# Performance work log

Measured on AMD Instinct MI355X. Metric: run time of the kernel, lower is better.

## Reference

```python
import math
import jax, jax.numpy as jnp
import numpy as np

HIDDEN = 768
NUM_HEADS = 12
HEAD_DIM = HIDDEN // NUM_HEADS
WINDOW = 256      # one-sided attention window
DILATION = 1
BATCH = 2
SEQ = 2048


def setup_inputs() -> dict:
    key = jax.random.key(0)
    ks = jax.random.split(key, 7)
    s = 1.0 / math.sqrt(HIDDEN)
    return {
        "hidden_states": jax.random.normal(ks[0], (BATCH, SEQ, HIDDEN), jnp.float32),
        "Wq": jax.random.normal(ks[1], (HIDDEN, HIDDEN), jnp.float32) * s,
        "bq": jnp.zeros((HIDDEN,), jnp.float32),
        "Wk": jax.random.normal(ks[2], (HIDDEN, HIDDEN), jnp.float32) * s,
        "bk": jnp.zeros((HIDDEN,), jnp.float32),
        "Wv": jax.random.normal(ks[3], (HIDDEN, HIDDEN), jnp.float32) * s,
        "bv": jnp.zeros((HIDDEN,), jnp.float32),
    }


def _band_mask(seq_len, dtype):
    # mask[i, j] = 1 iff |j - i| <= WINDOW * DILATION and (j - i) % DILATION == 0
    idx = jnp.arange(seq_len)
    rel = idx[None, :] - idx[:, None]  # [S, S]
    m = (jnp.abs(rel) <= WINDOW * DILATION) & (jnp.mod(rel, DILATION) == 0)
    return m.astype(dtype)


def reference(hidden_states, Wq, bq, Wk, bk, Wv, bv):
    B, S, M = hidden_states.shape
    H, D = NUM_HEADS, HEAD_DIM

    # torch nn.Linear: y = x @ W.T + b; query additionally scaled by 1/sqrt(head_dim)
    q = (hidden_states @ Wq.T + bq) / math.sqrt(D)
    k = hidden_states @ Wk.T + bk
    v = hidden_states @ Wv.T + bv

    # [B, S, M] -> [B, H, S, D]
    q = q.reshape(B, S, H, D).transpose(0, 2, 1, 3)
    k = k.reshape(B, S, H, D).transpose(0, 2, 1, 3)
    v = v.reshape(B, S, H, D).transpose(0, 2, 1, 3)

    # Dense scores, then MULTIPLICATIVE band mask (faithful: scores * mask, not additive -inf)
    scores = jnp.einsum("bhqd,bhkd->bhqk", q, k)
    mask = _band_mask(S, scores.dtype)  # [S, S], broadcasts over B, H
    scores = scores * mask

    probs = jax.nn.softmax(scores, axis=-1)  # [B, H, S, S]
    ctx = jnp.einsum("bhqk,bhkd->bhqd", probs, v)
    return ctx.transpose(0, 2, 1, 3).reshape(B, S, M)
```

## Files before the change

### kernel.cpp

```cpp
#include <hip/hip_runtime.h>
#include <hip/hip_bf16.h>
#include <cstdint>

#define SEQ    2048
#define HIDDEN 768
#define NHEAD  12
#define HDIM   64
#define WIN    256
#define BATCH  2
#define MTOT   (BATCH * SEQ)

typedef __attribute__((ext_vector_type(8))) short short8;
typedef __attribute__((ext_vector_type(4))) float f32x4;

__device__ __forceinline__ ushort bf16_rne(float f) {
    uint u = __float_as_uint(f);
    uint r = u + 0x7FFFu + ((u >> 16) & 1u);
    return (ushort)(r >> 16);
}
__device__ __forceinline__ float bf16_to_f(ushort h) {
    return __uint_as_float(((uint)h) << 16);
}

__global__ __launch_bounds__(256) void proj_mfma_kernel(
    const float* __restrict__ X,
    const float* __restrict__ Wq, const float* __restrict__ bq,
    const float* __restrict__ Wk, const float* __restrict__ bk,
    const float* __restrict__ Wv, const float* __restrict__ bv,
    float* __restrict__ Qo, float* __restrict__ Ko, float* __restrict__ Vo)
{
    const int which = blockIdx.z;
    const float* __restrict__ W    = (which == 0) ? Wq : (which == 1) ? Wk : Wv;
    const float* __restrict__ bias = (which == 0) ? bq : (which == 1) ? bk : bv;
    float* __restrict__ out        = (which == 0) ? Qo : (which == 1) ? Ko : Vo;
    const float scale = (which == 0) ? 0.125f : 1.0f;

    __shared__ __align__(16) ushort Ahi[128 * 64];
    __shared__ __align__(16) ushort Alo[128 * 64];
    __shared__ __align__(16) ushort Bhi[64 * 64];
    __shared__ __align__(16) ushort Blo[64 * 64];

    const int t  = threadIdx.x;
    const int m0 = blockIdx.x * 128;
    const int h  = blockIdx.y;
    const int n0 = h * 64;

    const int w    = t >> 6;
    const int lane = t & 63;
    const int wr   = w >> 1;
    const int wc   = w & 1;
    const int lr   = lane & 15;
    const int lk   = lane >> 4;

    f32x4 acc[4][2];
#pragma unroll
    for (int i = 0; i < 4; ++i)
#pragma unroll
        for (int j = 0; j < 2; ++j) acc[i][j] = (f32x4){0.f, 0.f, 0.f, 0.f};

    for (int k0 = 0; k0 < HIDDEN; k0 += 64) {
        __syncthreads();
#pragma unroll
        for (int i = 0; i < 8; ++i) {
            int id  = t + i * 256;
            int row = id >> 4;
            int c4  = id & 15;
            const float4 xv = *(const float4*)&X[(size_t)(m0 + row) * HIDDEN + k0 + c4 * 4];
            ushort h0 = bf16_rne(xv.x), h1 = bf16_rne(xv.y),
                   h2 = bf16_rne(xv.z), h3 = bf16_rne(xv.w);
            ushort l0 = bf16_rne(xv.x - bf16_to_f(h0)),
                   l1 = bf16_rne(xv.y - bf16_to_f(h1)),
                   l2 = bf16_rne(xv.z - bf16_to_f(h2)),
                   l3 = bf16_rne(xv.w - bf16_to_f(h3));
            int idx = (row * 64 + c4 * 4) ^ ((row & 7) << 3);
            *(uint2*)&Ahi[idx] = make_uint2((uint)h0 | ((uint)h1 << 16),
                                            (uint)h2 | ((uint)h3 << 16));
            *(uint2*)&Alo[idx] = make_uint2((uint)l0 | ((uint)l1 << 16),
                                            (uint)l2 | ((uint)l3 << 16));
        }
#pragma unroll
        for (int i = 0; i < 4; ++i) {
            int id  = t + i * 256;
            int row = id >> 4;
            int c4  = id & 15;
            const float4 wv4 = *(const float4*)&W[(size_t)(n0 + row) * HIDDEN + k0 + c4 * 4];
            ushort h0 = bf16_rne(wv4.x), h1 = bf16_rne(wv4.y),
                   h2 = bf16_rne(wv4.z), h3 = bf16_rne(wv4.w);
            ushort l0 = bf16_rne(wv4.x - bf16_to_f(h0)),
                   l1 = bf16_rne(wv4.y - bf16_to_f(h1)),
                   l2 = bf16_rne(wv4.z - bf16_to_f(h2)),
                   l3 = bf16_rne(wv4.w - bf16_to_f(h3));
            int idx = (row * 64 + c4 * 4) ^ ((row & 7) << 3);
            *(uint2*)&Bhi[idx] = make_uint2((uint)h0 | ((uint)h1 << 16),
                                            (uint)h2 | ((uint)h3 << 16));
            *(uint2*)&Blo[idx] = make_uint2((uint)l0 | ((uint)l1 << 16),
                                            (uint)l2 | ((uint)l3 << 16));
        }
        __syncthreads();

#pragma unroll
        for (int s = 0; s < 2; ++s) {
            short8 ah[4], al[4], bh[2], bl[2];
#pragma unroll
            for (int fm = 0; fm < 4; ++fm) {
                int row = wr * 64 + fm * 16 + lr;
                int idx = (row * 64 + s * 32 + lk * 8) ^ ((row & 7) << 3);
                ah[fm] = *(const short8*)&Ahi[idx];
                al[fm] = *(const short8*)&Alo[idx];
            }
#pragma unroll
            for (int fn = 0; fn < 2; ++fn) {
                int row = wc * 32 + fn * 16 + lr;
                int idx = (row * 64 + s * 32 + lk * 8) ^ ((row & 7) << 3);
                bh[fn] = *(const short8*)&Bhi[idx];
                bl[fn] = *(const short8*)&Blo[idx];
            }
#pragma unroll
            for (int fm = 0; fm < 4; ++fm)
#pragma unroll
                for (int fn = 0; fn < 2; ++fn) {
                    acc[fm][fn] = __builtin_amdgcn_mfma_f32_16x16x32_bf16(
                        ah[fm], bh[fn], acc[fm][fn], 0, 0, 0);
                    acc[fm][fn] = __builtin_amdgcn_mfma_f32_16x16x32_bf16(
                        ah[fm], bl[fn], acc[fm][fn], 0, 0, 0);
                    acc[fm][fn] = __builtin_amdgcn_mfma_f32_16x16x32_bf16(
                        al[fm], bh[fn], acc[fm][fn], 0, 0, 0);
                }
        }
    }

#pragma unroll
    for (int fn = 0; fn < 2; ++fn) {
        int d = wc * 32 + fn * 16 + lr;
        float bval = bias[n0 + d];
#pragma unroll
        for (int fm = 0; fm < 4; ++fm) {
#pragma unroll
            for (int r = 0; r < 4; ++r) {
                int m  = m0 + wr * 64 + fm * 16 + lk * 4 + r;
                int bb = m >> 11;
                int ss = m & (SEQ - 1);
                out[(((size_t)(bb * NHEAD + h) * SEQ) + ss) * HDIM + d] =
                    (acc[fm][fn][r] + bval) * scale;
            }
        }
    }
}

__global__ __launch_bounds__(256) void vprefix_kernel(
    const float* __restrict__ V, float* __restrict__ Vpre)
{
    const int bh    = blockIdx.x;
    const int d     = threadIdx.x & 63;
    const int chunk = threadIdx.x >> 6;
    const float* vb = &V[(size_t)bh * SEQ * HDIM];
    float* pb       = &Vpre[(size_t)bh * SEQ * HDIM];

    __shared__ float csum[4][64];
    const int s0 = chunk * 512;
    float sum = 0.f;
    for (int s = s0; s < s0 + 512; ++s) sum += vb[(size_t)s * HDIM + d];
    csum[chunk][d] = sum;
    __syncthreads();
    float run = 0.f;
    for (int c = 0; c < chunk; ++c) run += csum[c][d];
    for (int s = s0; s < s0 + 512; ++s) {
        run += vb[(size_t)s * HDIM + d];
        pb[(size_t)s * HDIM + d] = run;
    }
}

__global__ __launch_bounds__(256, 3) void attn_kernel(
    const float* __restrict__ Q, const float* __restrict__ K,
    const float* __restrict__ V, const float* __restrict__ Vpre,
    float* __restrict__ out)
{
    __shared__ __align__(16) ushort Khi[64 * 64], Klo[64 * 64];
    __shared__ __align__(16) ushort VThi[64 * 64], VTlo[64 * 64];
    __shared__ __align__(16) ushort Phi_s[4][16 * 64];
    __shared__ __align__(16) ushort Plo_s[4][16 * 64];

    const int t    = threadIdx.x;
    const int lane = t & 63;
    const int wv   = t >> 6;
    const int l15  = lane & 15;
    const int g2   = lane >> 4;

    const int L    = blockIdx.x;
    const int xcd  = L & 7;
    const int slot = L >> 3;
    const int bh   = xcd * 3 + (slot >> 5);
    const int qb   = slot & 31;
    const int b    = bh / NHEAD;
    const int h    = bh % NHEAD;
    const int i0   = qb * 64;
    const int i    = i0 + wv * 16 + l15;

    const float* kbase = &K[(size_t)bh * SEQ * HDIM];
    const float* vbase = &V[(size_t)bh * SEQ * HDIM];

    short8 qh[2], qlo[2];
    {
        const float* qrow = &Q[((size_t)bh * SEQ + i) * HDIM];
#pragma unroll
        for (int s = 0; s < 2; ++s) {
            float4 a = *(const float4*)&qrow[s * 32 + g2 * 8];
            float4 c = *(const float4*)&qrow[s * 32 + g2 * 8 + 4];
            float qf[8] = {a.x, a.y, a.z, a.w, c.x, c.y, c.z, c.w};
#pragma unroll
            for (int j = 0; j < 8; ++j) {
                ushort hh = bf16_rne(qf[j]);
                qh[s][j]  = (short)hh;
                qlo[s][j] = (short)bf16_rne(qf[j] - bf16_to_f(hh));
            }
        }
    }

    const int krow = t >> 2;
    const int kc   = (t & 3) * 16;
    const int vkp  = t >> 3;
    const int vdc  = (t & 7) * 8;
    float4 kpre[4], vp0[2], vp1[2];

    const int jlo_blk = max(0, i0 - WIN);
    const int jhi_blk = min(SEQ - 1, i0 + 63 + WIN);

    auto LOADT = [&](int jt2) {
        const float* kr = &kbase[(size_t)(jt2 + krow) * HDIM + kc];
        kpre[0] = *(const float4*)&kr[0];
        kpre[1] = *(const float4*)&kr[4];
        kpre[2] = *(const float4*)&kr[8];
        kpre[3] = *(const float4*)&kr[12];
        const float* vr0 = &vbase[(size_t)(jt2 + 2 * vkp) * HDIM + vdc];
        const float* vr1 = &vbase[(size_t)(jt2 + 2 * vkp + 1) * HDIM + vdc];
        vp0[0] = *(const float4*)&vr0[0];
        vp0[1] = *(const float4*)&vr0[4];
        vp1[0] = *(const float4*)&vr1[0];
        vp1[1] = *(const float4*)&vr1[4];
    };
    auto STORET = [&]() {
#pragma unroll
        for (int c = 0; c < 4; ++c) {
            float x0 = kpre[c].x, x1 = kpre[c].y, x2 = kpre[c].z, x3 = kpre[c].w;
            ushort h0 = bf16_rne(x0), h1 = bf16_rne(x1),
                   h2 = bf16_rne(x2), h3 = bf16_rne(x3);
            ushort l0 = bf16_rne(x0 - bf16_to_f(h0)),
                   l1 = bf16_rne(x1 - bf16_to_f(h1)),
                   l2 = bf16_rne(x2 - bf16_to_f(h2)),
                   l3 = bf16_rne(x3 - bf16_to_f(h3));
            int idx = (krow * 64 + kc + c * 4) ^ ((krow & 7) << 3);
            *(uint2*)&Khi[idx] = make_uint2((uint)h0 | ((uint)h1 << 16),
                                            (uint)h2 | ((uint)h3 << 16));
            *(uint2*)&Klo[idx] = make_uint2((uint)l0 | ((uint)l1 << 16),
                                            (uint)l2 | ((uint)l3 << 16));
        }
        float va[8] = {vp0[0].x, vp0[0].y, vp0[0].z, vp0[0].w,
                       vp0[1].x, vp0[1].y, vp0[1].z, vp0[1].w};
        float vb8[8] = {vp1[0].x, vp1[0].y, vp1[0].z, vp1[0].w,
                        vp1[1].x, vp1[1].y, vp1[1].z, vp1[1].w};
#pragma unroll
        for (int j = 0; j < 8; ++j) {
            int d = vdc + j;
            ushort ah = bf16_rne(va[j]), bh2 = bf16_rne(vb8[j]);
            ushort al = bf16_rne(va[j] - bf16_to_f(ah)),
                   bl = bf16_rne(vb8[j] - bf16_to_f(bh2));
            int idx = (d * 64 + 2 * vkp) ^ ((d & 7) << 3);
            *(uint*)&VThi[idx] = (uint)ah | ((uint)bh2 << 16);
            *(uint*)&VTlo[idx] = (uint)al | ((uint)bl << 16);
        }
    };

    float mrun = 0.f, lrun = 0.f;
    f32x4 ctx[4];
#pragma unroll
    for (int f = 0; f < 4; ++f) ctx[f] = (f32x4){0.f, 0.f, 0.f, 0.f};

    LOADT(jlo_blk);
    STORET();

    for (int jt = jlo_blk; jt <= jhi_blk; jt += 64) {
        const bool more = (jt + 64) <= jhi_blk;
        if (more) LOADT(jt + 64);
        __syncthreads();

        f32x4 sacc[4];
#pragma unroll
        for (int f = 0; f < 4; ++f) sacc[f] = (f32x4){0.f, 0.f, 0.f, 0.f};
#pragma unroll
        for (int s = 0; s < 2; ++s) {
            short8 kh[4], kl[4];
#pragma unroll
            for (int f = 0; f < 4; ++f) {
                int row = f * 16 + l15;
                int idx = (row * 64 + s * 32 + g2 * 8) ^ ((row & 7) << 3);
                kh[f] = *(const short8*)&Khi[idx];
                kl[f] = *(const short8*)&Klo[idx];
            }
#pragma unroll
            for (int f = 0; f < 4; ++f) {
                sacc[f] = __builtin_amdgcn_mfma_f32_16x16x32_bf16(kh[f], qh[s],  sacc[f], 0, 0, 0);
                sacc[f] = __builtin_amdgcn_mfma_f32_16x16x32_bf16(kh[f], qlo[s], sacc[f], 0, 0, 0);
                sacc[f] = __builtin_amdgcn_mfma_f32_16x16x32_bf16(kl[f], qh[s],  sacc[f], 0, 0, 0);
            }
        }

        float p[4][4];
        float tmax = -1e30f;
#pragma unroll
        for (int f = 0; f < 4; ++f)
#pragma unroll
            for (int r = 0; r < 4; ++r) {
                int j = jt + f * 16 + g2 * 4 + r;
                bool inw = (j >= i - WIN) && (j <= i + WIN);
                float sv_ = inw ? sacc[f][r] : -1e30f;
                p[f][r] = sv_;
                tmax = fmaxf(tmax, sv_);
            }
        tmax = fmaxf(tmax, __shfl_xor(tmax, 16));
        tmax = fmaxf(tmax, __shfl_xor(tmax, 32));
        float m_new = fmaxf(mrun, tmax);
        float resc  = __expf(mrun - m_new);
        float lsum  = 0.f;
#pragma unroll
        for (int f = 0; f < 4; ++f)
#pragma unroll
            for (int r = 0; r < 4; ++r) {
                float pe = __expf(p[f][r] - m_new);
                p[f][r] = pe;
                lsum += pe;
            }
        lsum += __shfl_xor(lsum, 16);
        lsum += __shfl_xor(lsum, 32);
        lrun = lrun * resc + lsum;
        mrun = m_new;
#pragma unroll
        for (int f = 0; f < 4; ++f) {
            ctx[f][0] *= resc; ctx[f][1] *= resc;
            ctx[f][2] *= resc; ctx[f][3] *= resc;
        }

#pragma unroll
        for (int f = 0; f < 4; ++f) {
            ushort h0 = bf16_rne(p[f][0]), h1 = bf16_rne(p[f][1]),
                   h2 = bf16_rne(p[f][2]), h3 = bf16_rne(p[f][3]);
            ushort l0 = bf16_rne(p[f][0] - bf16_to_f(h0)),
                   l1 = bf16_rne(p[f][1] - bf16_to_f(h1)),
                   l2 = bf16_rne(p[f][2] - bf16_to_f(h2)),
                   l3 = bf16_rne(p[f][3] - bf16_to_f(h3));
            int idx = (l15 * 64 + f * 16 + g2 * 4) ^ ((l15 & 7) << 3);
            *(uint2*)&Phi_s[wv][idx] = make_uint2((uint)h0 | ((uint)h1 << 16),
                                                  (uint)h2 | ((uint)h3 << 16));
            *(uint2*)&Plo_s[wv][idx] = make_uint2((uint)l0 | ((uint)l1 << 16),
                                                  (uint)l2 | ((uint)l3 << 16));
        }

#pragma unroll
        for (int s = 0; s < 2; ++s) {
            int pidx = (l15 * 64 + s * 32 + g2 * 8) ^ ((l15 & 7) << 3);
            short8 ph = *(const short8*)&Phi_s[wv][pidx];
            short8 pl = *(const short8*)&Plo_s[wv][pidx];
#pragma unroll
            for (int f = 0; f < 4; ++f) {
                int row = f * 16 + l15;
                int idx = (row * 64 + s * 32 + g2 * 8) ^ ((row & 7) << 3);
                short8 vh = *(const short8*)&VThi[idx];
                short8 vl = *(const short8*)&VTlo[idx];
                ctx[f] = __builtin_amdgcn_mfma_f32_16x16x32_bf16(vh, ph, ctx[f], 0, 0, 0);
                ctx[f] = __builtin_amdgcn_mfma_f32_16x16x32_bf16(vl, ph, ctx[f], 0, 0, 0);
                ctx[f] = __builtin_amdgcn_mfma_f32_16x16x32_bf16(vh, pl, ctx[f], 0, 0, 0);
            }
        }

        __syncthreads();
        if (more) STORET();
    }

    const int jlo = max(0, i - WIN);
    const int jhi = min(SEQ - 1, i + WIN);
    const int cnt = jhi - jlo + 1;
    const float em   = __expf(-mrun);
    const float ltot = lrun + (float)(SEQ - cnt) * em;
    const float inv  = 1.f / ltot;

    const float* vpT = &Vpre[((size_t)bh * SEQ + (SEQ - 1)) * HDIM];
    const float* vpH = &Vpre[((size_t)bh * SEQ + jhi) * HDIM];
    const float* vpL = &Vpre[((size_t)bh * SEQ + (jlo - 1)) * HDIM];
    float* orow = &out[((size_t)(b * SEQ + i)) * HIDDEN + h * HDIM];

#pragma unroll
    for (int f = 0; f < 4; ++f) {
        int d0 = f * 16 + g2 * 4;
        float4 tt = *(const float4*)&vpT[d0];
        float4 hh = *(const float4*)&vpH[d0];
        float4 ll = {0.f, 0.f, 0.f, 0.f};
        if (jlo > 0) ll = *(const float4*)&vpL[d0];
        float4 o;
        o.x = (ctx[f][0] + em * (tt.x - hh.x + ll.x)) * inv;
        o.y = (ctx[f][1] + em * (tt.y - hh.y + ll.y)) * inv;
        o.z = (ctx[f][2] + em * (tt.z - hh.z + ll.z)) * inv;
        o.w = (ctx[f][3] + em * (tt.w - hh.w + ll.w)) * inv;
        *(float4*)&orow[d0] = o;
    }
}

extern "C" void kernel_launch(void* const* d_in, const int* in_sizes, int n_in,
                              void* d_out, int out_size, void* d_ws, size_t ws_size,
                              hipStream_t stream) {
    const float* X  = (const float*)d_in[0];
    const float* Wq = (const float*)d_in[1];
    const float* bq = (const float*)d_in[2];
    const float* Wk = (const float*)d_in[3];
    const float* bk = (const float*)d_in[4];
    const float* Wv = (const float*)d_in[5];
    const float* bv = (const float*)d_in[6];
    float* out = (float*)d_out;

    const size_t TEN = (size_t)BATCH * NHEAD * SEQ * HDIM;
    float* qf   = (float*)d_ws;
    float* kf   = qf + TEN;
    float* vf   = kf + TEN;
    float* vpre = vf + TEN;

    proj_mfma_kernel<<<dim3(MTOT / 128, NHEAD, 3), 256, 0, stream>>>(
        X, Wq, bq, Wk, bk, Wv, bv, qf, kf, vf);
    vprefix_kernel<<<dim3(BATCH * NHEAD), 256, 0, stream>>>(vf, vpre);
    attn_kernel<<<dim3((SEQ / 64) * BATCH * NHEAD), 256, 0, stream>>>(
        qf, kf, vf, vpre, out);
}
```

Baseline: 259.6 us.

## Pre-split tensors into bf16 hi/lo in global memory with transposed V

Adds a conversion kernel that splits X and the weights into bf16 hi/lo pairs once, up front. The projection now writes Q, K and V directly as hi/lo bf16, with V stored transposed (head-dim major). The attention kernel can then copy K and V tiles straight into shared memory, instead of re-converting fp32 on every tile load. The V prefix-sum kernel is rewritten for the transposed layout with more threads and vector loads, and its output reuses the X workspace region. The cost is extra launches and global traffic for the conversion, scalar ushort stores in the Q/K epilogue, and strided per-element prefix reads in the attention epilogue.

```diff
diff --git a/kernel.cpp b/kernel.cpp
--- a/kernel.cpp
+++ b/kernel.cpp
@@ -22,18 +22,38 @@
     return __uint_as_float(((uint)h) << 16);
 }
 
+__global__ __launch_bounds__(256) void convert_kernel(
+    const float* __restrict__ src, ushort* __restrict__ hi,
+    ushort* __restrict__ lo, int n4)
+{
+    int id = blockIdx.x * 256 + threadIdx.x;
+    if (id >= n4) return;
+    float4 v = ((const float4*)src)[id];
+    ushort h0 = bf16_rne(v.x), h1 = bf16_rne(v.y),
+           h2 = bf16_rne(v.z), h3 = bf16_rne(v.w);
+    ushort l0 = bf16_rne(v.x - bf16_to_f(h0)),
+           l1 = bf16_rne(v.y - bf16_to_f(h1)),
+           l2 = bf16_rne(v.z - bf16_to_f(h2)),
+           l3 = bf16_rne(v.w - bf16_to_f(h3));
+    *(uint2*)&hi[(size_t)id * 4] = make_uint2((uint)h0 | ((uint)h1 << 16),
+                                              (uint)h2 | ((uint)h3 << 16));
+    *(uint2*)&lo[(size_t)id * 4] = make_uint2((uint)l0 | ((uint)l1 << 16),
+                                              (uint)l2 | ((uint)l3 << 16));
+}
+
 __global__ __launch_bounds__(256) void proj_mfma_kernel(
-    const float* __restrict__ X,
-    const float* __restrict__ Wq, const float* __restrict__ bq,
-    const float* __restrict__ Wk, const float* __restrict__ bk,
-    const float* __restrict__ Wv, const float* __restrict__ bv,
-    float* __restrict__ Qo, float* __restrict__ Ko, float* __restrict__ Vo)
+    const ushort* __restrict__ Xhi, const ushort* __restrict__ Xlo,
+    const ushort* __restrict__ Whi, const ushort* __restrict__ Wlo,
+    const float* __restrict__ bq, const float* __restrict__ bk,
+    const float* __restrict__ bv,
+    ushort* __restrict__ Qhi, ushort* __restrict__ Qlo,
+    ushort* __restrict__ Khi_g, ushort* __restrict__ Klo_g,
+    ushort* __restrict__ VThi_g, ushort* __restrict__ VTlo_g)
 {
     const int which = blockIdx.z;
-    const float* __restrict__ W    = (which == 0) ? Wq : (which == 1) ? Wk : Wv;
     const float* __restrict__ bias = (which == 0) ? bq : (which == 1) ? bk : bv;
-    float* __restrict__ out        = (which == 0) ? Qo : (which == 1) ? Ko : Vo;
     const float scale = (which == 0) ? 0.125f : 1.0f;
+    const size_t woff = (size_t)which * 768 * 768;
 
     __shared__ __align__(16) ushort Ahi[128 * 64];
     __shared__ __align__(16) ushort Alo[128 * 64];
@@ -52,6 +72,9 @@
     const int lr   = lane & 15;
     const int lk   = lane >> 4;
 
+    const int srow = t >> 3;
+    const int sc8  = t & 7;
+
     f32x4 acc[4][2];
 #pragma unroll
     for (int i = 0; i < 4; ++i)
@@ -59,48 +82,41 @@
         for (int j = 0; j < 2; ++j) acc[i][j] = (f32x4){0.f, 0.f, 0.f, 0.f};
 
     for (int k0 = 0; k0 < HIDDEN; k0 += 64) {
+        uint4 a_h[4], a_l[4], b_h[2], b_l[2];
+#pragma unroll
+        for (int i = 0; i < 4; ++i) {
+            int row = srow + i * 32;
+            size_t g = (size_t)(m0 + row) * HIDDEN + k0 + sc8 * 8;
+            a_h[i] = *(const uint4*)&Xhi[g];
+            a_l[i] = *(const uint4*)&Xlo[g];
+        }
+#pragma unroll
+        for (int i = 0; i < 2; ++i) {
+            int row = srow + i * 32;
+            size_t g = woff + (size_t)(n0 + row) * HIDDEN + k0 + sc8 * 8;
+            b_h[i] = *(const uint4*)&Whi[g];
+            b_l[i] = *(const uint4*)&Wlo[g];
+        }
         __syncthreads();
 #pragma unroll
-        for (int i = 0; i < 8; ++i) {
-            int id  = t + i * 256;
-            int row = id >> 4;
-            int c4  = id & 15;
-            const float4 xv = *(const float4*)&X[(size_t)(m0 + row) * HIDDEN + k0 + c4 * 4];
-            ushort h0 = bf16_rne(xv.x), h1 = bf16_rne(xv.y),
-                   h2 = bf16_rne(xv.z), h3 = bf16_rne(xv.w);
-            ushort l0 = bf16_rne(xv.x - bf16_to_f(h0)),
-                   l1 = bf16_rne(xv.y - bf16_to_f(h1)),
-                   l2 = bf16_rne(xv.z - bf16_to_f(h2)),
-                   l3 = bf16_rne(xv.w - bf16_to_f(h3));
-            int idx = (row * 64 + c4 * 4) ^ ((row & 7) << 3);
-            *(uint2*)&Ahi[idx] = make_uint2((uint)h0 | ((uint)h1 << 16),
-                                            (uint)h2 | ((uint)h3 << 16));
-            *(uint2*)&Alo[idx] = make_uint2((uint)l0 | ((uint)l1 << 16),
-                                            (uint)l2 | ((uint)l3 << 16));
-        }
-#pragma unroll
         for (int i = 0; i < 4; ++i) {
-            int id  = t + i * 256;
-            int row = id >> 4;
-            int c4  = id & 15;
-            const float4 wv4 = *(const float4*)&W[(size_t)(n0 + row) * HIDDEN + k0 + c4 * 4];
-            ushort h0 = bf16_rne(wv4.x), h1 = bf16_rne(wv4.y),
-                   h2 = bf16_rne(wv4.z), h3 = bf16_rne(wv4.w);
-            ushort l0 = bf16_rne(wv4.x - bf16_to_f(h0)),
-                   l1 = bf16_rne(wv4.y - bf16_to_f(h1)),
-                   l2 = bf16_rne(wv4.z - bf16_to_f(h2)),
-                   l3 = bf16_rne(wv4.w - bf16_to_f(h3));
-            int idx = (row * 64 + c4 * 4) ^ ((row & 7) << 3);
-            *(uint2*)&Bhi[idx] = make_uint2((uint)h0 | ((uint)h1 << 16),
-                                            (uint)h2 | ((uint)h3 << 16));
-            *(uint2*)&Blo[idx] = make_uint2((uint)l0 | ((uint)l1 << 16),
-                                            (uint)l2 | ((uint)l3 << 16));
+            int row = srow + i * 32;
+            int idx = (row * 64 + sc8 * 8) ^ ((row & 7) << 3);
+            *(uint4*)&Ahi[idx] = a_h[i];
+            *(uint4*)&Alo[idx] = a_l[i];
+        }
+#pragma unroll
+        for (int i = 0; i < 2; ++i) {
+            int row = srow + i * 32;
+            int idx = (row * 64 + sc8 * 8) ^ ((row & 7) << 3);
+            *(uint4*)&Bhi[idx] = b_h[i];
+            *(uint4*)&Blo[idx] = b_l[i];
         }
         __syncthreads();
 
 #pragma unroll
         for (int s = 0; s < 2; ++s) {
-            short8 ah[4], al[4], bh[2], bl[2];
+            short8 ah[4], al[4], bh2[2], bl2[2];
 #pragma unroll
             for (int fm = 0; fm < 4; ++fm) {
                 int row = wr * 64 + fm * 16 + lr;
@@ -112,68 +128,130 @@
             for (int fn = 0; fn < 2; ++fn) {
                 int row = wc * 32 + fn * 16 + lr;
                 int idx = (row * 64 + s * 32 + lk * 8) ^ ((row & 7) << 3);
-                bh[fn] = *(const short8*)&Bhi[idx];
-                bl[fn] = *(const short8*)&Blo[idx];
+                bh2[fn] = *(const short8*)&Bhi[idx];
+                bl2[fn] = *(const short8*)&Blo[idx];
             }
 #pragma unroll
             for (int fm = 0; fm < 4; ++fm)
 #pragma unroll
                 for (int fn = 0; fn < 2; ++fn) {
                     acc[fm][fn] = __builtin_amdgcn_mfma_f32_16x16x32_bf16(
-                        ah[fm], bh[fn], acc[fm][fn], 0, 0, 0);
+                        ah[fm], bh2[fn], acc[fm][fn], 0, 0, 0);
                     acc[fm][fn] = __builtin_amdgcn_mfma_f32_16x16x32_bf16(
-                        ah[fm], bl[fn], acc[fm][fn], 0, 0, 0);
+                        ah[fm], bl2[fn], acc[fm][fn], 0, 0, 0);
                     acc[fm][fn] = __builtin_amdgcn_mfma_f32_16x16x32_bf16(
-                        al[fm], bh[fn], acc[fm][fn], 0, 0, 0);
+                        al[fm], bh2[fn], acc[fm][fn], 0, 0, 0);
                 }
         }
     }
 
-#pragma unroll
-    for (int fn = 0; fn < 2; ++fn) {
-        int d = wc * 32 + fn * 16 + lr;
-        float bval = bias[n0 + d];
-#pragma unroll
-        for (int fm = 0; fm < 4; ++fm) {
-#pragma unroll
-            for (int r = 0; r < 4; ++r) {
-                int m  = m0 + wr * 64 + fm * 16 + lk * 4 + r;
+    if (which == 2) {
+#pragma unroll
+        for (int fn = 0; fn < 2; ++fn) {
+            int d = wc * 32 + fn * 16 + lr;
+            float bval = bias[n0 + d];
+#pragma unroll
+            for (int fm = 0; fm < 4; ++fm) {
+                int m  = m0 + wr * 64 + fm * 16 + lk * 4;
                 int bb = m >> 11;
                 int ss = m & (SEQ - 1);
-                out[(((size_t)(bb * NHEAD + h) * SEQ) + ss) * HDIM + d] =
-                    (acc[fm][fn][r] + bval) * scale;
-            }
-        }
-    }
-}
-
-__global__ __launch_bounds__(256) void vprefix_kernel(
-    const float* __restrict__ V, float* __restrict__ Vpre)
+                ushort hs[4], ls[4];
+#pragma unroll
+                for (int r = 0; r < 4; ++r) {
+                    float val = acc[fm][fn][r] + bval;
+                    hs[r] = bf16_rne(val);
+                    ls[r] = bf16_rne(val - bf16_to_f(hs[r]));
+                }
+                size_t base = ((size_t)(bb * NHEAD + h) * HDIM + d) * SEQ + ss;
+                *(uint2*)&VThi_g[base] = make_uint2((uint)hs[0] | ((uint)hs[1] << 16),
+                                                    (uint)hs[2] | ((uint)hs[3] << 16));
+                *(uint2*)&VTlo_g[base] = make_uint2((uint)ls[0] | ((uint)ls[1] << 16),
+                                                    (uint)ls[2] | ((uint)ls[3] << 16));
+            }
+        }
+    } else {
+        ushort* __restrict__ ohi = (which == 0) ? Qhi : Khi_g;
+        ushort* __restrict__ olo = (which == 0) ? Qlo : Klo_g;
+#pragma unroll
+        for (int fn = 0; fn < 2; ++fn) {
+            int d = wc * 32 + fn * 16 + lr;
+            float bval = bias[n0 + d];
+#pragma unroll
+            for (int fm = 0; fm < 4; ++fm) {
+#pragma unroll
+                for (int r = 0; r < 4; ++r) {
+                    int m  = m0 + wr * 64 + fm * 16 + lk * 4 + r;
+                    int bb = m >> 11;
+                    int ss = m & (SEQ - 1);
+                    float val = (acc[fm][fn][r] + bval) * scale;
+                    ushort hh = bf16_rne(val);
+                    ushort ll = bf16_rne(val - bf16_to_f(hh));
+                    size_t base = ((size_t)(bb * NHEAD + h) * SEQ + ss) * HDIM + d;
+                    ohi[base] = hh;
+                    olo[base] = ll;
+                }
+            }
+        }
+    }
+}
+
+__global__ __launch_bounds__(1024) void vprefix_kernel(
+    const ushort* __restrict__ VThi_g, const ushort* __restrict__ VTlo_g,
+    float* __restrict__ vpre)
 {
-    const int bh    = blockIdx.x;
-    const int d     = threadIdx.x & 63;
-    const int chunk = threadIdx.x >> 6;
-    const float* vb = &V[(size_t)bh * SEQ * HDIM];
-    float* pb       = &Vpre[(size_t)bh * SEQ * HDIM];
-
-    __shared__ float csum[4][64];
-    const int s0 = chunk * 512;
+    const int bh = blockIdx.x;
+    const int d  = threadIdx.x >> 4;
+    const int c  = threadIdx.x & 15;
+    const size_t base = ((size_t)bh * HDIM + d) * SEQ + c * 128;
+    const ushort* ph = &VThi_g[base];
+    const ushort* pl = &VTlo_g[base];
+
+    __shared__ float csum[64][16];
     float sum = 0.f;
-    for (int s = s0; s < s0 + 512; ++s) sum += vb[(size_t)s * HDIM + d];
-    csum[chunk][d] = sum;
+#pragma unroll 4
+    for (int s8 = 0; s8 < 16; ++s8) {
+        uint4 H = *(const uint4*)&ph[s8 * 8];
+        uint4 L = *(const uint4*)&pl[s8 * 8];
+        sum += bf16_to_f((ushort)(H.x & 0xFFFF)) + bf16_to_f((ushort)(L.x & 0xFFFF));
+        sum += bf16_to_f((ushort)(H.x >> 16))    + bf16_to_f((ushort)(L.x >> 16));
+        sum += bf16_to_f((ushort)(H.y & 0xFFFF)) + bf16_to_f((ushort)(L.y & 0xFFFF));
+        sum += bf16_to_f((ushort)(H.y >> 16))    + bf16_to_f((ushort)(L.y >> 16));
+        sum += bf16_to_f((ushort)(H.z & 0xFFFF)) + bf16_to_f((ushort)(L.z & 0xFFFF));
+        sum += bf16_to_f((ushort)(H.z >> 16))    + bf16_to_f((ushort)(L.z >> 16));
+        sum += bf16_to_f((ushort)(H.w & 0xFFFF)) + bf16_to_f((ushort)(L.w & 0xFFFF));
+        sum += bf16_to_f((ushort)(H.w >> 16))    + bf16_to_f((ushort)(L.w >> 16));
+    }
+    csum[d][c] = sum;
     __syncthreads();
     float run = 0.f;
-    for (int c = 0; c < chunk; ++c) run += csum[c][d];
-    for (int s = s0; s < s0 + 512; ++s) {
-        run += vb[(size_t)s * HDIM + d];
-        pb[(size_t)s * HDIM + d] = run;
+    for (int cc = 0; cc < c; ++cc) run += csum[d][cc];
+
+    float* po = &vpre[base];
+    for (int s8 = 0; s8 < 16; ++s8) {
+        uint4 H = *(const uint4*)&ph[s8 * 8];
+        uint4 L = *(const uint4*)&pl[s8 * 8];
+        float f[8];
+        f[0] = bf16_to_f((ushort)(H.x & 0xFFFF)) + bf16_to_f((ushort)(L.x & 0xFFFF));
+        f[1] = bf16_to_f((ushort)(H.x >> 16))    + bf16_to_f((ushort)(L.x >> 16));
+        f[2] = bf16_to_f((ushort)(H.y & 0xFFFF)) + bf16_to_f((ushort)(L.y & 0xFFFF));
+        f[3] = bf16_to_f((ushort)(H.y >> 16))    + bf16_to_f((ushort)(L.y >> 16));
+        f[4] = bf16_to_f((ushort)(H.z & 0xFFFF)) + bf16_to_f((ushort)(L.z & 0xFFFF));
+        f[5] = bf16_to_f((ushort)(H.z >> 16))    + bf16_to_f((ushort)(L.z >> 16));
+        f[6] = bf16_to_f((ushort)(H.w & 0xFFFF)) + bf16_to_f((ushort)(L.w & 0xFFFF));
+        f[7] = bf16_to_f((ushort)(H.w >> 16))    + bf16_to_f((ushort)(L.w >> 16));
+        float buf[8];
+#pragma unroll
+        for (int j = 0; j < 8; ++j) { run += f[j]; buf[j] = run; }
+        *(float4*)&po[s8 * 8]     = make_float4(buf[0], buf[1], buf[2], buf[3]);
+        *(float4*)&po[s8 * 8 + 4] = make_float4(buf[4], buf[5], buf[6], buf[7]);
     }
 }
 
 __global__ __launch_bounds__(256, 3) void attn_kernel(
-    const float* __restrict__ Q, const float* __restrict__ K,
-    const float* __restrict__ V, const float* __restrict__ Vpre,
-    float* __restrict__ out)
+    const ushort* __restrict__ Qhi_g, const ushort* __restrict__ Qlo_g,
+    const ushort* __restrict__ Khi_g, const ushort* __restrict__ Klo_g,
+    const ushort* __restrict__ VThi_g, const ushort* __restrict__ VTlo_g,
+    const float* __restrict__ vpre, float* __restrict__ out)
 {
     __shared__ __align__(16) ushort Khi[64 * 64], Klo[64 * 64];
     __shared__ __align__(16) ushort VThi[64 * 64], VTlo[64 * 64];
@@ -196,77 +274,48 @@
     const int i0   = qb * 64;
     const int i    = i0 + wv * 16 + l15;
 
-    const float* kbase = &K[(size_t)bh * SEQ * HDIM];
-    const float* vbase = &V[(size_t)bh * SEQ * HDIM];
-
     short8 qh[2], qlo[2];
     {
-        const float* qrow = &Q[((size_t)bh * SEQ + i) * HDIM];
+        const size_t qb_ = ((size_t)bh * SEQ + i) * HDIM;
 #pragma unroll
         for (int s = 0; s < 2; ++s) {
-            float4 a = *(const float4*)&qrow[s * 32 + g2 * 8];
-            float4 c = *(const float4*)&qrow[s * 32 + g2 * 8 + 4];
-            float qf[8] = {a.x, a.y, a.z, a.w, c.x, c.y, c.z, c.w};
-#pragma unroll
-            for (int j = 0; j < 8; ++j) {
-                ushort hh = bf16_rne(qf[j]);
-                qh[s][j]  = (short)hh;
-                qlo[s][j] = (short)bf16_rne(qf[j] - bf16_to_f(hh));
-            }
-        }
-    }
-
-    const int krow = t >> 2;
-    const int kc   = (t & 3) * 16;
-    const int vkp  = t >> 3;
-    const int vdc  = (t & 7) * 8;
-    float4 kpre[4], vp0[2], vp1[2];
+            qh[s]  = *(const short8*)&Qhi_g[qb_ + s * 32 + g2 * 8];
+            qlo[s] = *(const short8*)&Qlo_g[qb_ + s * 32 + g2 * 8];
+        }
+    }
+
+    const int srow = t >> 3;
+    const int sc8  = t & 7;
+    uint4 kh_p[2], kl_p[2], vh_p[2], vl_p[2];
 
     const int jlo_blk = max(0, i0 - WIN);
     const int jhi_blk = min(SEQ - 1, i0 + 63 + WIN);
 
     auto LOADT = [&](int jt2) {
-        const float* kr = &kbase[(size_t)(jt2 + krow) * HDIM + kc];
-        kpre[0] = *(const float4*)&kr[0];
-        kpre[1] = *(const float4*)&kr[4];
-        kpre[2] = *(const float4*)&kr[8];
-        kpre[3] = *(const float4*)&kr[12];
-        const float* vr0 = &vbase[(size_t)(jt2 + 2 * vkp) * HDIM + vdc];
-        const float* vr1 = &vbase[(size_t)(jt2 + 2 * vkp + 1) * HDIM + vdc];
-        vp0[0] = *(const float4*)&vr0[0];
-        vp0[1] = *(const float4*)&vr0[4];
-        vp1[0] = *(const float4*)&vr1[0];
-        vp1[1] = *(const float4*)&vr1[4];
+        const size_t kb = ((size_t)bh * SEQ + jt2) * HDIM;
+#pragma unroll
+        for (int u = 0; u < 2; ++u) {
+            size_t g = kb + (size_t)(srow + u * 32) * HDIM + sc8 * 8;
+            kh_p[u] = *(const uint4*)&Khi_g[g];
+            kl_p[u] = *(const uint4*)&Klo_g[g];
+        }
+        const size_t vb = (size_t)bh * HDIM * SEQ + jt2;
+#pragma unroll
+        for (int u = 0; u < 2; ++u) {
+            size_t g = vb + (size_t)(srow + u * 32) * SEQ + sc8 * 8;
+            vh_p[u] = *(const uint4*)&VThi_g[g];
+            vl_p[u] = *(const uint4*)&VTlo_g[g];
+        }
     };
     auto STORET = [&]() {
 #pragma unroll
-        for (int c = 0; c < 4; ++c) {
-            float x0 = kpre[c].x, x1 = kpre[c].y, x2 = kpre[c].z, x3 = kpre[c].w;
-            ushort h0 = bf16_rne(x0), h1 = bf16_rne(x1),
-                   h2 = bf16_rne(x2), h3 = bf16_rne(x3);
-            ushort l0 = bf16_rne(x0 - bf16_to_f(h0)),
-                   l1 = bf16_rne(x1 - bf16_to_f(h1)),
-                   l2 = bf16_rne(x2 - bf16_to_f(h2)),
-                   l3 = bf16_rne(x3 - bf16_to_f(h3));
-            int idx = (krow * 64 + kc + c * 4) ^ ((krow & 7) << 3);
-            *(uint2*)&Khi[idx] = make_uint2((uint)h0 | ((uint)h1 << 16),
-                                            (uint)h2 | ((uint)h3 << 16));
-            *(uint2*)&Klo[idx] = make_uint2((uint)l0 | ((uint)l1 << 16),
-                                            (uint)l2 | ((uint)l3 << 16));
-        }
-        float va[8] = {vp0[0].x, vp0[0].y, vp0[0].z, vp0[0].w,
-                       vp0[1].x, vp0[1].y, vp0[1].z, vp0[1].w};
-        float vb8[8] = {vp1[0].x, vp1[0].y, vp1[0].z, vp1[0].w,
-                        vp1[1].x, vp1[1].y, vp1[1].z, vp1[1].w};
-#pragma unroll
-        for (int j = 0; j < 8; ++j) {
-            int d = vdc + j;
-            ushort ah = bf16_rne(va[j]), bh2 = bf16_rne(vb8[j]);
-            ushort al = bf16_rne(va[j] - bf16_to_f(ah)),
-                   bl = bf16_rne(vb8[j] - bf16_to_f(bh2));
-            int idx = (d * 64 + 2 * vkp) ^ ((d & 7) << 3);
-            *(uint*)&VThi[idx] = (uint)ah | ((uint)bh2 << 16);
-            *(uint*)&VTlo[idx] = (uint)al | ((uint)bl << 16);
+        for (int u = 0; u < 2; ++u) {
+            int row = srow + u * 32;
+            int idx = (row * 64 + sc8 * 8) ^ ((row & 7) << 3);
+            *(uint4*)&Khi[idx]  = kh_p[u];
+            *(uint4*)&Klo[idx]  = kl_p[u];
+            *(uint4*)&VThi[idx] = vh_p[u];
+            *(uint4*)&VTlo[idx] = vl_p[u];
         }
     };
 
@@ -382,24 +431,20 @@
     const float ltot = lrun + (float)(SEQ - cnt) * em;
     const float inv  = 1.f / ltot;
 
-    const float* vpT = &Vpre[((size_t)bh * SEQ + (SEQ - 1)) * HDIM];
-    const float* vpH = &Vpre[((size_t)bh * SEQ + jhi) * HDIM];
-    const float* vpL = &Vpre[((size_t)bh * SEQ + (jlo - 1)) * HDIM];
     float* orow = &out[((size_t)(b * SEQ + i)) * HIDDEN + h * HDIM];
-
 #pragma unroll
     for (int f = 0; f < 4; ++f) {
         int d0 = f * 16 + g2 * 4;
-        float4 tt = *(const float4*)&vpT[d0];
-        float4 hh = *(const float4*)&vpH[d0];
-        float4 ll = {0.f, 0.f, 0.f, 0.f};
-        if (jlo > 0) ll = *(const float4*)&vpL[d0];
-        float4 o;
-        o.x = (ctx[f][0] + em * (tt.x - hh.x + ll.x)) * inv;
-        o.y = (ctx[f][1] + em * (tt.y - hh.y + ll.y)) * inv;
-        o.z = (ctx[f][2] + em * (tt.z - hh.z + ll.z)) * inv;
-        o.w = (ctx[f][3] + em * (tt.w - hh.w + ll.w)) * inv;
-        *(float4*)&orow[d0] = o;
+        float o[4];
+#pragma unroll
+        for (int j = 0; j < 4; ++j) {
+            const float* ch = &vpre[((size_t)bh * HDIM + d0 + j) * SEQ];
+            float tt = ch[SEQ - 1];
+            float hh = ch[jhi];
+            float ll = (jlo > 0) ? ch[jlo - 1] : 0.f;
+            o[j] = (ctx[f][j] + em * (tt - hh + ll)) * inv;
+        }
+        *(float4*)&orow[d0] = make_float4(o[0], o[1], o[2], o[3]);
     }
 }
 
@@ -415,15 +460,32 @@
     const float* bv = (const float*)d_in[6];
     float* out = (float*)d_out;
 
-    const size_t TEN = (size_t)BATCH * NHEAD * SEQ * HDIM;
-    float* qf   = (float*)d_ws;
-    float* kf   = qf + TEN;
-    float* vf   = kf + TEN;
-    float* vpre = vf + TEN;
+    const size_t NX = (size_t)MTOT * HIDDEN;
+    const size_t NW = (size_t)HIDDEN * HIDDEN;
+    const size_t NT = (size_t)BATCH * NHEAD * SEQ * HDIM;
+
+    ushort* Xhi  = (ushort*)d_ws;
+    ushort* Xlo  = Xhi  + NX;
+    ushort* Whi  = Xlo  + NX;
+    ushort* Wlo  = Whi  + 3 * NW;
+    ushort* Qhi  = Wlo  + 3 * NW;
+    ushort* Qlo  = Qhi  + NT;
+    ushort* Khi  = Qlo  + NT;
+    ushort* Klo  = Khi  + NT;
+    ushort* VThi = Klo  + NT;
+    ushort* VTlo = VThi + NT;
+    float*  vpre = (float*)d_ws;
+
+    convert_kernel<<<(int)(NX / 4 / 256), 256, 0, stream>>>(X, Xhi, Xlo, (int)(NX / 4));
+    convert_kernel<<<(int)(NW / 4 / 256), 256, 0, stream>>>(Wq, Whi, Wlo, (int)(NW / 4));
+    convert_kernel<<<(int)(NW / 4 / 256), 256, 0, stream>>>(Wk, Whi + NW, Wlo + NW, (int)(NW / 4));
+    convert_kernel<<<(int)(NW / 4 / 256), 256, 0, stream>>>(Wv, Whi + 2 * NW, Wlo + 2 * NW, (int)(NW / 4));
 
     proj_mfma_kernel<<<dim3(MTOT / 128, NHEAD, 3), 256, 0, stream>>>(
-        X, Wq, bq, Wk, bk, Wv, bv, qf, kf, vf);
-    vprefix_kernel<<<dim3(BATCH * NHEAD), 256, 0, stream>>>(vf, vpre);
+        Xhi, Xlo, Whi, Wlo, bq, bk, bv, Qhi, Qlo, Khi, Klo, VThi, VTlo);
+
+    vprefix_kernel<<<dim3(BATCH * NHEAD), 1024, 0, stream>>>(VThi, VTlo, vpre);
+
     attn_kernel<<<dim3((SEQ / 64) * BATCH * NHEAD), 256, 0, stream>>>(
-        qf, kf, vf, vpre, out);
-}
+        Qhi, Qlo, Khi, Klo, VThi, VTlo, vpre, out);
+}
```

Result: slower. 431.0 us (+66.1%).

## Fuse QKV projections per block and double attention query tile to 128 rows

Applied to the files above, without the earlier changes.

The projection kernel now computes Q, K and V for the same 128-row X tile in one block. The X tile is converted to hi/lo bf16 once instead of three times, at the cost of three times more accumulator registers and larger weight LDS buffers. The attention kernel moves to 512-thread blocks covering 128 query rows, so each K/V tile loaded and converted is shared across twice as many queries. The trade-off is half as many blocks and more LDS for P, which may hurt occupancy and grid fill.

```diff
diff --git a/kernel.cpp b/kernel.cpp
--- a/kernel.cpp
+++ b/kernel.cpp
@@ -29,16 +29,10 @@
     const float* __restrict__ Wv, const float* __restrict__ bv,
     float* __restrict__ Qo, float* __restrict__ Ko, float* __restrict__ Vo)
 {
-    const int which = blockIdx.z;
-    const float* __restrict__ W    = (which == 0) ? Wq : (which == 1) ? Wk : Wv;
-    const float* __restrict__ bias = (which == 0) ? bq : (which == 1) ? bk : bv;
-    float* __restrict__ out        = (which == 0) ? Qo : (which == 1) ? Ko : Vo;
-    const float scale = (which == 0) ? 0.125f : 1.0f;
-
     __shared__ __align__(16) ushort Ahi[128 * 64];
     __shared__ __align__(16) ushort Alo[128 * 64];
-    __shared__ __align__(16) ushort Bhi[64 * 64];
-    __shared__ __align__(16) ushort Blo[64 * 64];
+    __shared__ __align__(16) ushort Bhi[3 * 64 * 64];
+    __shared__ __align__(16) ushort Blo[3 * 64 * 64];
 
     const int t  = threadIdx.x;
     const int m0 = blockIdx.x * 128;
@@ -52,11 +46,15 @@
     const int lr   = lane & 15;
     const int lk   = lane >> 4;
 
-    f32x4 acc[4][2];
-#pragma unroll
-    for (int i = 0; i < 4; ++i)
-#pragma unroll
-        for (int j = 0; j < 2; ++j) acc[i][j] = (f32x4){0.f, 0.f, 0.f, 0.f};
+    const float* const Wp[3] = {Wq, Wk, Wv};
+
+    f32x4 acc[3][4][2];
+#pragma unroll
+    for (int q = 0; q < 3; ++q)
+#pragma unroll
+        for (int i = 0; i < 4; ++i)
+#pragma unroll
+            for (int j = 0; j < 2; ++j) acc[q][i][j] = (f32x4){0.f, 0.f, 0.f, 0.f};
 
     for (int k0 = 0; k0 < HIDDEN; k0 += 64) {
         __syncthreads();
@@ -79,28 +77,32 @@
                                             (uint)l2 | ((uint)l3 << 16));
         }
 #pragma unroll
-        for (int i = 0; i < 4; ++i) {
-            int id  = t + i * 256;
-            int row = id >> 4;
-            int c4  = id & 15;
-            const float4 wv4 = *(const float4*)&W[(size_t)(n0 + row) * HIDDEN + k0 + c4 * 4];
-            ushort h0 = bf16_rne(wv4.x), h1 = bf16_rne(wv4.y),
-                   h2 = bf16_rne(wv4.z), h3 = bf16_rne(wv4.w);
-            ushort l0 = bf16_rne(wv4.x - bf16_to_f(h0)),
-                   l1 = bf16_rne(wv4.y - bf16_to_f(h1)),
-                   l2 = bf16_rne(wv4.z - bf16_to_f(h2)),
-                   l3 = bf16_rne(wv4.w - bf16_to_f(h3));
-            int idx = (row * 64 + c4 * 4) ^ ((row & 7) << 3);
-            *(uint2*)&Bhi[idx] = make_uint2((uint)h0 | ((uint)h1 << 16),
-                                            (uint)h2 | ((uint)h3 << 16));
-            *(uint2*)&Blo[idx] = make_uint2((uint)l0 | ((uint)l1 << 16),
-                                            (uint)l2 | ((uint)l3 << 16));
+        for (int q = 0; q < 3; ++q) {
+            const float* __restrict__ Wb = Wp[q];
+#pragma unroll
+            for (int i = 0; i < 4; ++i) {
+                int id  = t + i * 256;
+                int row = id >> 4;
+                int c4  = id & 15;
+                const float4 wv4 = *(const float4*)&Wb[(size_t)(n0 + row) * HIDDEN + k0 + c4 * 4];
+                ushort h0 = bf16_rne(wv4.x), h1 = bf16_rne(wv4.y),
+                       h2 = bf16_rne(wv4.z), h3 = bf16_rne(wv4.w);
+                ushort l0 = bf16_rne(wv4.x - bf16_to_f(h0)),
+                       l1 = bf16_rne(wv4.y - bf16_to_f(h1)),
+                       l2 = bf16_rne(wv4.z - bf16_to_f(h2)),
+                       l3 = bf16_rne(wv4.w - bf16_to_f(h3));
+                int idx = q * 4096 + ((row * 64 + c4 * 4) ^ ((row & 7) << 3));
+                *(uint2*)&Bhi[idx] = make_uint2((uint)h0 | ((uint)h1 << 16),
+                                                (uint)h2 | ((uint)h3 << 16));
+                *(uint2*)&Blo[idx] = make_uint2((uint)l0 | ((uint)l1 << 16),
+                                                (uint)l2 | ((uint)l3 << 16));
+            }
         }
         __syncthreads();
 
 #pragma unroll
         for (int s = 0; s < 2; ++s) {
-            short8 ah[4], al[4], bh[2], bl[2];
+            short8 ah[4], al[4];
 #pragma unroll
             for (int fm = 0; fm < 4; ++fm) {
                 int row = wr * 64 + fm * 16 + lr;
@@ -109,39 +111,49 @@
                 al[fm] = *(const short8*)&Alo[idx];
             }
 #pragma unroll
-            for (int fn = 0; fn < 2; ++fn) {
-                int row = wc * 32 + fn * 16 + lr;
-                int idx = (row * 64 + s * 32 + lk * 8) ^ ((row & 7) << 3);
-                bh[fn] = *(const short8*)&Bhi[idx];
-                bl[fn] = *(const short8*)&Blo[idx];
-            }
-#pragma unroll
-            for (int fm = 0; fm < 4; ++fm)
+            for (int q = 0; q < 3; ++q) {
+                short8 bh2[2], bl2[2];
 #pragma unroll
                 for (int fn = 0; fn < 2; ++fn) {
-                    acc[fm][fn] = __builtin_amdgcn_mfma_f32_16x16x32_bf16(
-                        ah[fm], bh[fn], acc[fm][fn], 0, 0, 0);
-                    acc[fm][fn] = __builtin_amdgcn_mfma_f32_16x16x32_bf16(
-                        ah[fm], bl[fn], acc[fm][fn], 0, 0, 0);
-                    acc[fm][fn] = __builtin_amdgcn_mfma_f32_16x16x32_bf16(
-                        al[fm], bh[fn], acc[fm][fn], 0, 0, 0);
+                    int row = wc * 32 + fn * 16 + lr;
+                    int idx = q * 4096 + ((row * 64 + s * 32 + lk * 8) ^ ((row & 7) << 3));
+                    bh2[fn] = *(const short8*)&Bhi[idx];
+                    bl2[fn] = *(const short8*)&Blo[idx];
                 }
-        }
-    }
-
-#pragma unroll
-    for (int fn = 0; fn < 2; ++fn) {
-        int d = wc * 32 + fn * 16 + lr;
-        float bval = bias[n0 + d];
-#pragma unroll
-        for (int fm = 0; fm < 4; ++fm) {
-#pragma unroll
-            for (int r = 0; r < 4; ++r) {
-                int m  = m0 + wr * 64 + fm * 16 + lk * 4 + r;
-                int bb = m >> 11;
-                int ss = m & (SEQ - 1);
-                out[(((size_t)(bb * NHEAD + h) * SEQ) + ss) * HDIM + d] =
-                    (acc[fm][fn][r] + bval) * scale;
+#pragma unroll
+                for (int fm = 0; fm < 4; ++fm)
+#pragma unroll
+                    for (int fn = 0; fn < 2; ++fn) {
+                        acc[q][fm][fn] = __builtin_amdgcn_mfma_f32_16x16x32_bf16(
+                            ah[fm], bh2[fn], acc[q][fm][fn], 0, 0, 0);
+                        acc[q][fm][fn] = __builtin_amdgcn_mfma_f32_16x16x32_bf16(
+                            ah[fm], bl2[fn], acc[q][fm][fn], 0, 0, 0);
+                        acc[q][fm][fn] = __builtin_amdgcn_mfma_f32_16x16x32_bf16(
+                            al[fm], bh2[fn], acc[q][fm][fn], 0, 0, 0);
+                    }
+            }
+        }
+    }
+
+#pragma unroll
+    for (int q = 0; q < 3; ++q) {
+        const float* __restrict__ bias = (q == 0) ? bq : (q == 1) ? bk : bv;
+        float* __restrict__ out        = (q == 0) ? Qo : (q == 1) ? Ko : Vo;
+        const float scale = (q == 0) ? 0.125f : 1.0f;
+#pragma unroll
+        for (int fn = 0; fn < 2; ++fn) {
+            int d = wc * 32 + fn * 16 + lr;
+            float bval = bias[n0 + d];
+#pragma unroll
+            for (int fm = 0; fm < 4; ++fm) {
+#pragma unroll
+                for (int r = 0; r < 4; ++r) {
+                    int m  = m0 + wr * 64 + fm * 16 + lk * 4 + r;
+                    int bb = m >> 11;
+                    int ss = m & (SEQ - 1);
+                    out[(((size_t)(bb * NHEAD + h) * SEQ) + ss) * HDIM + d] =
+                        (acc[q][fm][fn][r] + bval) * scale;
+                }
             }
         }
     }
@@ -170,15 +182,15 @@
     }
 }
 
-__global__ __launch_bounds__(256, 3) void attn_kernel(
+__global__ __launch_bounds__(512, 2) void attn_kernel(
     const float* __restrict__ Q, const float* __restrict__ K,
     const float* __restrict__ V, const float* __restrict__ Vpre,
     float* __restrict__ out)
 {
     __shared__ __align__(16) ushort Khi[64 * 64], Klo[64 * 64];
     __shared__ __align__(16) ushort VThi[64 * 64], VTlo[64 * 64];
-    __shared__ __align__(16) ushort Phi_s[4][16 * 64];
-    __shared__ __align__(16) ushort Plo_s[4][16 * 64];
+    __shared__ __align__(16) ushort Phi_s[8][16 * 64];
+    __shared__ __align__(16) ushort Plo_s[8][16 * 64];
 
     const int t    = threadIdx.x;
     const int lane = t & 63;
@@ -189,11 +201,11 @@
     const int L    = blockIdx.x;
     const int xcd  = L & 7;
     const int slot = L >> 3;
-    const int bh   = xcd * 3 + (slot >> 5);
-    const int qb   = slot & 31;
+    const int bh   = xcd * 3 + (slot >> 4);
+    const int qb   = slot & 15;
     const int b    = bh / NHEAD;
     const int h    = bh % NHEAD;
-    const int i0   = qb * 64;
+    const int i0   = qb * 128;
     const int i    = i0 + wv * 16 + l15;
 
     const float* kbase = &K[(size_t)bh * SEQ * HDIM];
@@ -216,31 +228,25 @@
         }
     }
 
-    const int krow = t >> 2;
-    const int kc   = (t & 3) * 16;
-    const int vkp  = t >> 3;
-    const int vdc  = (t & 7) * 8;
-    float4 kpre[4], vp0[2], vp1[2];
+    const int krow = t >> 3;
+    const int kc   = (t & 7) * 8;
+    const int vkp  = t >> 4;
+    const int vdc  = (t & 15) * 4;
+    float4 kpre[2], vp0, vp1;
 
     const int jlo_blk = max(0, i0 - WIN);
-    const int jhi_blk = min(SEQ - 1, i0 + 63 + WIN);
+    const int jhi_blk = min(SEQ - 1, i0 + 127 + WIN);
 
     auto LOADT = [&](int jt2) {
         const float* kr = &kbase[(size_t)(jt2 + krow) * HDIM + kc];
         kpre[0] = *(const float4*)&kr[0];
         kpre[1] = *(const float4*)&kr[4];
-        kpre[2] = *(const float4*)&kr[8];
-        kpre[3] = *(const float4*)&kr[12];
-        const float* vr0 = &vbase[(size_t)(jt2 + 2 * vkp) * HDIM + vdc];
-        const float* vr1 = &vbase[(size_t)(jt2 + 2 * vkp + 1) * HDIM + vdc];
-        vp0[0] = *(const float4*)&vr0[0];
-        vp0[1] = *(const float4*)&vr0[4];
-        vp1[0] = *(const float4*)&vr1[0];
-        vp1[1] = *(const float4*)&vr1[4];
+        vp0 = *(const float4*)&vbase[(size_t)(jt2 + 2 * vkp) * HDIM + vdc];
+        vp1 = *(const float4*)&vbase[(size_t)(jt2 + 2 * vkp + 1) * HDIM + vdc];
     };
     auto STORET = [&]() {
 #pragma unroll
-        for (int c = 0; c < 4; ++c) {
+        for (int c = 0; c < 2; ++c) {
             float x0 = kpre[c].x, x1 = kpre[c].y, x2 = kpre[c].z, x3 = kpre[c].w;
             ushort h0 = bf16_rne(x0), h1 = bf16_rne(x1),
                    h2 = bf16_rne(x2), h3 = bf16_rne(x3);
@@ -254,16 +260,14 @@
             *(uint2*)&Klo[idx] = make_uint2((uint)l0 | ((uint)l1 << 16),
                                             (uint)l2 | ((uint)l3 << 16));
         }
-        float va[8] = {vp0[0].x, vp0[0].y, vp0[0].z, vp0[0].w,
-                       vp0[1].x, vp0[1].y, vp0[1].z, vp0[1].w};
-        float vb8[8] = {vp1[0].x, vp1[0].y, vp1[0].z, vp1[0].w,
-                        vp1[1].x, vp1[1].y, vp1[1].z, vp1[1].w};
-#pragma unroll
-        for (int j = 0; j < 8; ++j) {
+        float va[4] = {vp0.x, vp0.y, vp0.z, vp0.w};
+        float vb4[4] = {vp1.x, vp1.y, vp1.z, vp1.w};
+#pragma unroll
+        for (int j = 0; j < 4; ++j) {
             int d = vdc + j;
-            ushort ah = bf16_rne(va[j]), bh2 = bf16_rne(vb8[j]);
+            ushort ah = bf16_rne(va[j]), bh2 = bf16_rne(vb4[j]);
             ushort al = bf16_rne(va[j] - bf16_to_f(ah)),
-                   bl = bf16_rne(vb8[j] - bf16_to_f(bh2));
+                   bl = bf16_rne(vb4[j] - bf16_to_f(bh2));
             int idx = (d * 64 + 2 * vkp) ^ ((d & 7) << 3);
             *(uint*)&VThi[idx] = (uint)ah | ((uint)bh2 << 16);
             *(uint*)&VTlo[idx] = (uint)al | ((uint)bl << 16);
@@ -421,9 +425,9 @@
     float* vf   = kf + TEN;
     float* vpre = vf + TEN;
 
-    proj_mfma_kernel<<<dim3(MTOT / 128, NHEAD, 3), 256, 0, stream>>>(
+    proj_mfma_kernel<<<dim3(MTOT / 128, NHEAD), 256, 0, stream>>>(
         X, Wq, bq, Wk, bk, Wv, bv, qf, kf, vf);
     vprefix_kernel<<<dim3(BATCH * NHEAD), 256, 0, stream>>>(vf, vpre);
-    attn_kernel<<<dim3((SEQ / 64) * BATCH * NHEAD), 256, 0, stream>>>(
+    attn_kernel<<<dim3((SEQ / 128) * BATCH * NHEAD), 512, 0, stream>>>(
         qf, kf, vf, vpre, out);
 }
```

New measurement: 379.1 us. +46.1%, slower.
